# Kernel tuning notes

Hardware: AMD Instinct MI355X
Metric: run time of the kernel (lower is better)

## Reference

```python
import jax, jax.numpy as jnp
import numpy as np

B, S, D, K = 8, 2048, 1024, 204  # K = int(0.1 * seq_len)
LN_EPS = 1e-12


def setup_inputs() -> dict:
    key = jax.random.key(0)
    ks = jax.random.split(key, 8)
    scale = 0.02
    return {
        "input_tensor": jax.random.normal(ks[0], (B, S, D), jnp.float32),
        "attention_mask": jnp.zeros((B, 1, 1, S), jnp.float32),  # unused by module
        "Wq": jax.random.normal(ks[1], (D, K), jnp.float32) * scale,
        "bq": jnp.zeros((K,), jnp.float32),
        "Wk": jax.random.normal(ks[2], (D, K), jnp.float32) * scale,
        "bk": jnp.zeros((K,), jnp.float32),
        "Wv": jax.random.normal(ks[3], (D, D), jnp.float32) * scale,
        "bv": jnp.zeros((D,), jnp.float32),
        "Wd": jax.random.normal(ks[4], (D, D), jnp.float32) * scale,
        "bd": jnp.zeros((D,), jnp.float32),
        "gamma": jnp.ones((D,), jnp.float32),
        "beta": jnp.zeros((D,), jnp.float32),
    }


def reference(input_tensor, attention_mask, Wq, bq, Wk, bk, Wv, bv, Wd, bd, gamma, beta):
    # factorized synthesizer: low-rank (k=204) Q/K projections
    q = input_tensor @ Wq + bq          # [B,S,K]
    k = input_tensor @ Wk + bk          # [B,S,K]
    v = input_tensor @ Wv + bv          # [B,S,D]
    scores = jnp.einsum('bsk,btk->bst', q, k)          # [B,S,S]
    probs = jax.nn.softmax(scores, axis=-1)
    # per-head matmul with broadcast probs == direct matmul on merged heads
    ctx = jnp.einsum('bst,btd->bsd', probs, v)          # [B,S,D]
    h = ctx @ Wd + bd
    y = h + input_tensor                                 # residual
    mean = jnp.mean(y, axis=-1, keepdims=True)
    var = jnp.mean(jnp.square(y - mean), axis=-1, keepdims=True)
    return gamma * (y - mean) / jnp.sqrt(var + LN_EPS) + beta
```

## Files before the change

kernel.cpp:

```cpp
#include <hip/hip_runtime.h>
#include <stdint.h>

#define BB 8
#define SS 2048
#define DD 1024
#define KREAL 204

typedef __attribute__((ext_vector_type(8))) short short8;
typedef __attribute__((ext_vector_type(4))) float floatx4;
typedef uint16_t u16;
typedef uint32_t u32;

__device__ __forceinline__ float bf2f(u16 u) {
    union { float f; u32 i; } c; c.i = ((u32)u) << 16; return c.f;
}
__device__ __forceinline__ u16 f2bf(float f) {
    union { float f; u32 i; } c; c.f = f;
    u32 i = c.i;
    u32 r = (i + 0x7FFFu + ((i >> 16) & 1u)) >> 16;
    return (u16)r;
}

#if defined(__has_builtin)
#if __has_builtin(__builtin_amdgcn_global_load_lds)
#define HAVE_GLL 1
#endif
#endif

__device__ __forceinline__ void gload16(const u16* g, u16* l) {
#ifdef HAVE_GLL
    __builtin_amdgcn_global_load_lds(
        (const __attribute__((address_space(1))) void*)(uintptr_t)g,
        (__attribute__((address_space(3))) void*)(u32)(uintptr_t)(void*)l,
        16, 0, 0);
#else
    *(uint4*)l = *(const uint4*)g;
#endif
}

#define VM_WAIT(N) asm volatile("s_waitcnt vmcnt(" #N ")" ::: "memory")
#define S_BAR()    asm volatile("s_barrier" ::: "memory")

__device__ __forceinline__ void stage64(const u16* __restrict__ src, size_t ld,
                                        u16* lds, int tid) {
#pragma unroll
    for (int j = 0; j < 2; j++) {
        int flat = j * 256 + tid;
        int row = flat >> 3, slot = flat & 7;
        int kg = slot ^ (row & 7);
        gload16(src + (size_t)row * ld + kg * 8, lds + flat * 8);
    }
}
__device__ __forceinline__ short8 frag(const u16* lds, int row, int kslot) {
    return *(const short8*)&lds[(row << 6) + (((kslot ^ (row & 7)) & 7) << 3)];
}

__device__ __forceinline__ short8 frag32(const u16* plane, int row, int ks) {
    return *(const short8*)&plane[(row << 5) + (((ks ^ ((row >> 1) & 3)) & 3) << 3)];
}

__device__ __forceinline__ void stage_half(const u16* s0, const u16* s1,
                                           u16* dp, int tid) {
    gload16(s0, dp + tid * 8);
    gload16(s1, dp + 4096 + tid * 8);
}

template <int MT, bool LOADB>
__device__ __forceinline__ void phase16(const u16* Apl, const u16* Bpl,
                                        int arow, int brow, int ln, int quad,
                                        short8 (&bv)[4], floatx4 (&acc)[8][4]) {
    short8 af[4];
#pragma unroll
    for (int i = 0; i < 4; i++) af[i] = frag32(Apl, arow + (MT + i) * 16 + ln, quad);
    if (LOADB) {
#pragma unroll
        for (int nt = 0; nt < 4; nt++) bv[nt] = frag32(Bpl, brow + nt * 16 + ln, quad);
    }
    __builtin_amdgcn_s_setprio(1);
#pragma unroll
    for (int i = 0; i < 4; i++)
#pragma unroll
        for (int nt = 0; nt < 4; nt++)
            acc[MT + i][nt] = __builtin_amdgcn_mfma_f32_16x16x32_bf16(
                af[i], bv[nt], acc[MT + i][nt], 0, 0, 0);
    __builtin_amdgcn_s_setprio(0);
}

template <int NT>
__device__ __forceinline__ void gemm_core256(
    const u16* __restrict__ Ag, size_t lda,
    const u16* __restrict__ Bg, size_t ldb,
    u16* lds, int tid, floatx4 (&acc)[8][4]) {
    const int lane = tid & 63, w = tid >> 6;
    const int arow = (w >> 2) * 128, brow = (w & 3) * 64;
    const int ln = lane & 15, quad = lane >> 4;
    const int srow = tid >> 2;
    const int kgp = (tid & 3) ^ ((srow >> 1) & 3);
    const u16* A0 = Ag + (size_t)srow * lda + kgp * 8;
    const u16* A1 = Ag + (size_t)(srow + 128) * lda + kgp * 8;
    const u16* B0 = Bg + (size_t)srow * ldb + kgp * 8;
    const u16* B1 = Bg + (size_t)(srow + 128) * ldb + kgp * 8;
    u16* Al = lds;
    u16* Bl = lds + 32768;

    stage_half(A0,      A1,      Al,         tid);
    stage_half(B0,      B1,      Bl,         tid);
    stage_half(A0 + 32, A1 + 32, Al + 8192,  tid);
    stage_half(B0 + 32, B1 + 32, Bl + 8192,  tid);
    stage_half(A0 + 64, A1 + 64, Al + 16384, tid);
    stage_half(B0 + 64, B1 + 64, Bl + 16384, tid);

    short8 bv[4];
#pragma unroll 2
    for (int t = 0; t < NT - 1; ++t) {
        const int p  = (t & 1) * 2;
        const int pn = 2 - p;
        const u16* Ap0 = Al + p * 8192;
        const u16* Ap1 = Al + p * 8192 + 8192;
        const u16* Bp0 = Bl + p * 8192;
        const u16* Bp1 = Bl + p * 8192 + 8192;
        const size_t o1 = (size_t)(t + 1) * 64;
        const size_t o2 = (size_t)(t + 2) * 64;
        VM_WAIT(8); S_BAR();
        stage_half(A0 + o1 + 32, A1 + o1 + 32, Al + (pn + 1) * 8192, tid);
        phase16<0, true >(Ap0, Bp0, arow, brow, ln, quad, bv, acc);
        stage_half(B0 + o1 + 32, B1 + o1 + 32, Bl + (pn + 1) * 8192, tid);
        phase16<4, false>(Ap0, Bp0, arow, brow, ln, quad, bv, acc);
        VM_WAIT(8); S_BAR();
        if (t + 2 < NT) stage_half(A0 + o2, A1 + o2, Al + p * 8192, tid);
        phase16<0, true >(Ap1, Bp1, arow, brow, ln, quad, bv, acc);
        if (t + 2 < NT) stage_half(B0 + o2, B1 + o2, Bl + p * 8192, tid);
        phase16<4, false>(Ap1, Bp1, arow, brow, ln, quad, bv, acc);
    }
    {
        const int p = ((NT - 1) & 1) * 2;
        const u16* Ap0 = Al + p * 8192;
        const u16* Ap1 = Al + p * 8192 + 8192;
        const u16* Bp0 = Bl + p * 8192;
        const u16* Bp1 = Bl + p * 8192 + 8192;
        VM_WAIT(4); S_BAR();
        phase16<0, true >(Ap0, Bp0, arow, brow, ln, quad, bv, acc);
        phase16<4, false>(Ap0, Bp0, arow, brow, ln, quad, bv, acc);
        VM_WAIT(0); S_BAR();
        phase16<0, true >(Ap1, Bp1, arow, brow, ln, quad, bv, acc);
        phase16<4, false>(Ap1, Bp1, arow, brow, ln, quad, bv, acc);
    }
}

template <typename F>
__device__ __forceinline__ void store_rm256(u16* smem, u16* gbase, size_t ldc,
                                            int wm, int wn, int ln, int quad,
                                            int tid, F val) {
    for (int half = 0; half < 2; half++) {
        __syncthreads();
        if (wm == half) {
#pragma unroll
            for (int mt = 0; mt < 8; mt++)
#pragma unroll
                for (int nt = 0; nt < 4; nt++)
#pragma unroll
                    for (int r = 0; r < 4; r++)
                        smem[(mt * 16 + quad * 4 + r) * 264 + wn * 64 + nt * 16 + ln] =
                            val(mt, nt, r);
        }
        __syncthreads();
#pragma unroll
        for (int j = 0; j < 8; j++) {
            int flat = j * 512 + tid;
            int row = flat >> 5, c = flat & 31;
            *(uint4*)&gbase[(size_t)(half * 128 + row) * ldc + c * 8] =
                *(const uint4*)&smem[row * 264 + c * 8];
        }
    }
}

template <typename F4>
__device__ __forceinline__ void store_tr256(u16* smem, u16* gbase, size_t ldg,
                                            int wm, int wn, int ln, int quad,
                                            int tid, F4 val4) {
    for (int qr = 0; qr < 4; qr++) {
        __syncthreads();
        if (wn == qr) {
#pragma unroll
            for (int mt = 0; mt < 8; mt++)
#pragma unroll
                for (int nt = 0; nt < 4; nt++) {
                    ushort4 v = val4(mt, nt);
                    *(ushort4*)&smem[(nt * 16 + ln) * 264 + wm * 128 + mt * 16 + quad * 4] = v;
                }
        }
        __syncthreads();
#pragma unroll
        for (int j = 0; j < 4; j++) {
            int flat = j * 512 + tid;
            int c = flat >> 5, r8 = flat & 31;
            *(uint4*)&gbase[(size_t)(qr * 64 + c) * ldg + r8 * 8] =
                *(const uint4*)&smem[c * 264 + r8 * 8];
        }
    }
}

__global__ __launch_bounds__(256) void k_cast_bf16(
    const float* __restrict__ x, u16* __restrict__ o) {
    size_t i = ((size_t)blockIdx.x * 256 + threadIdx.x) * 4;
    float4 v = *(const float4*)&x[i];
    ushort4 p;
    p.x = f2bf(v.x); p.y = f2bf(v.y); p.z = f2bf(v.z); p.w = f2bf(v.w);
    *(ushort4*)&o[i] = p;
}

__global__ __launch_bounds__(256) void k_prep(
    const float* __restrict__ Wq, const float* __restrict__ Wk,
    const float* __restrict__ Wv, const float* __restrict__ Wd,
    const float* __restrict__ bv, const float* __restrict__ bd,
    const float* __restrict__ bq, const float* __restrict__ bk,
    u16* __restrict__ Wqkt, u16* __restrict__ Wv16, u16* __restrict__ Wdt,
    float* __restrict__ bc, float* __restrict__ bqk) {
    const int z = blockIdx.z;
    const int t = threadIdx.x;
    if (z == 4) {
        int id = blockIdx.y * 32 + blockIdx.x;
        if (id < 16) {
            __shared__ float red[4][64];
            int n = id * 64 + (t & 63);
            int dc = t >> 6;
            float s = 0.f;
            for (int d = dc * 256; d < dc * 256 + 256; d++)
                s += bv[d] * Wd[(size_t)d * 1024 + n];
            red[dc][t & 63] = s;
            __syncthreads();
            if (dc == 0) bc[n] = bd[n] + red[0][t & 63] + red[1][t & 63] + red[2][t & 63] + red[3][t & 63];
        } else if (id == 16) {
            for (int i = t; i < 512; i += 256) {
                float v = 0.f;
                if (i < KREAL) v = bq[i];
                else if (i >= 256 && i < 256 + KREAL) v = bk[i - 256];
                bqk[i] = v;
            }
        }
        return;
    }
    __shared__ u16 tile[32][33];
    int k0 = blockIdx.x * 32, n0 = blockIdx.y * 32;
    int tx = t & 31, ty = t >> 5;
    if (z == 2) {
        for (int i = ty; i < 32; i += 8) {
            size_t idx = (size_t)(k0 + i) * 1024 + n0 + tx;
            Wv16[idx] = f2bf(Wv[idx]);
        }
        return;
    }
    const float* W; u16* out; int N, Npad, rowoff;
    if (z == 0)      { W = Wq; out = Wqkt; N = KREAL; Npad = 256;  rowoff = 0;   }
    else if (z == 1) { W = Wk; out = Wqkt; N = KREAL; Npad = 256;  rowoff = 256; }
    else             { W = Wd; out = Wdt;  N = 1024;  Npad = 1024; rowoff = 0;   }
    if (n0 >= Npad) return;
    for (int i = ty; i < 32; i += 8) {
        int n = n0 + tx;
        tile[i][tx] = (n < N) ? f2bf(W[(size_t)(k0 + i) * N + n]) : (u16)0;
    }
    __syncthreads();
    for (int i = ty; i < 32; i += 8) {
        int n = n0 + i;
        if (n < Npad) out[(size_t)(rowoff + n) * 1024 + k0 + tx] = tile[tx][i];
    }
}

__global__ __launch_bounds__(256) void k_gemm64(
    const u16* __restrict__ A, const u16* __restrict__ Bt,
    u16* __restrict__ C, int ldc) {
    __shared__ u16 As[64 * 64];
    __shared__ u16 Bs[64 * 64];
    const int tid = threadIdx.x;
    const int m0 = blockIdx.x * 64, n0 = blockIdx.y * 64;
    const int lane = tid & 63, w = tid >> 6;
    const int ln = lane & 15, quad = lane >> 4;

    floatx4 acc[4];
    floatx4 zero = {0.f, 0.f, 0.f, 0.f};
#pragma unroll
    for (int nt = 0; nt < 4; nt++) acc[nt] = zero;

    for (int kt = 0; kt < 16; kt++) {
        __syncthreads();
        stage64(A + (size_t)m0 * 1024 + kt * 64, 1024, As, tid);
        stage64(Bt + (size_t)n0 * 1024 + kt * 64, 1024, Bs, tid);
        __syncthreads();
#pragma unroll
        for (int kk = 0; kk < 2; kk++) {
            short8 av = frag(As, w * 16 + ln, kk * 4 + quad);
#pragma unroll
            for (int nt = 0; nt < 4; nt++) {
                short8 bvf = frag(Bs, nt * 16 + ln, kk * 4 + quad);
                acc[nt] = __builtin_amdgcn_mfma_f32_16x16x32_bf16(av, bvf, acc[nt], 0, 0, 0);
            }
        }
    }
    const int row0 = m0 + w * 16 + quad * 4;
#pragma unroll
    for (int nt = 0; nt < 4; nt++) {
        const int col = n0 + nt * 16 + ln;
        ushort4 pk;
        pk.x = f2bf(acc[nt][0]); pk.y = f2bf(acc[nt][1]);
        pk.z = f2bf(acc[nt][2]); pk.w = f2bf(acc[nt][3]);
        *reinterpret_cast<ushort4*>(&C[(size_t)col * ldc + row0]) = pk;
    }
}

__global__ __launch_bounds__(512, 2) void k_proj2(
    const u16* __restrict__ A, const u16* __restrict__ Wqkt,
    const u16* __restrict__ Wvdt, const float* __restrict__ bqk,
    u16* __restrict__ qkp, u16* __restrict__ ut) {
    __shared__ __align__(16) u16 lds[65536];
    const int tid = threadIdx.x;
    int lin = blockIdx.x + (blockIdx.y << 6);
    int l = (lin & 7) * 48 + (lin >> 3);
    const int by = l % 6;
    const int m0 = (l / 6) * 256;
    const int lane = tid & 63, w = tid >> 6;
    const int wm = w >> 2, wn = w & 3;
    const int ln = lane & 15, quad = lane >> 4;

    floatx4 acc[8][4];
    floatx4 zero = {0.f, 0.f, 0.f, 0.f};
#pragma unroll
    for (int mt = 0; mt < 8; mt++)
#pragma unroll
        for (int nt = 0; nt < 4; nt++) acc[mt][nt] = zero;

    const u16* Ag = A + (size_t)m0 * 1024;
    const int n0 = (by < 2) ? by * 256 : (by - 2) * 256;
    const u16* Bg = (by < 2) ? (Wqkt + (size_t)n0 * 1024) : (Wvdt + (size_t)n0 * 1024);
    gemm_core256<16>(Ag, 1024, Bg, 1024, lds, tid, acc);

    if (by < 2) {
        float b4[4];
#pragma unroll
        for (int nt = 0; nt < 4; nt++) b4[nt] = bqk[n0 + wn * 64 + nt * 16 + ln];
        store_rm256(lds, qkp + (size_t)m0 * 512 + n0, 512, wm, wn, ln, quad, tid,
            [&](int mt, int nt, int r) -> u16 {
                return f2bf(acc[mt][nt][r] + b4[nt]);
            });
    } else {
        int b = m0 >> 11, s0loc = m0 & 2047;
        store_tr256(lds, ut + ((size_t)b * DD + n0) * SS + s0loc, SS, wm, wn, ln, quad, tid,
            [&](int mt, int nt) -> ushort4 {
                ushort4 pk;
                pk.x = f2bf(acc[mt][nt][0]); pk.y = f2bf(acc[mt][nt][1]);
                pk.z = f2bf(acc[mt][nt][2]); pk.w = f2bf(acc[mt][nt][3]);
                return pk;
            });
    }
}

__global__ __launch_bounds__(512, 2) void k_qk2(
    const u16* __restrict__ qkp, u16* __restrict__ P, float* __restrict__ lg) {
    __shared__ __align__(16) u16 lds[65536];
    const int tid = threadIdx.x;
    int lin = blockIdx.x + (blockIdx.y << 3) + (blockIdx.z << 6);
    int l = ((lin & 7) << 6) + (lin >> 3);
    const int bb = l >> 6, rem = l & 63;
    const int s0 = (rem & 7) * 256, t0 = (rem >> 3) * 256;
    const int lane = tid & 63, w = tid >> 6;
    const int wm = w >> 2, wn = w & 3;
    const int ln = lane & 15, quad = lane >> 4;

    floatx4 acc[8][4];
    floatx4 zero = {0.f, 0.f, 0.f, 0.f};
#pragma unroll
    for (int mt = 0; mt < 8; mt++)
#pragma unroll
        for (int nt = 0; nt < 4; nt++) acc[mt][nt] = zero;

    gemm_core256<4>(qkp + ((size_t)bb * SS + s0) * 512, 512,
                    qkp + ((size_t)bb * SS + t0) * 512 + 256, 512, lds, tid, acc);

#pragma unroll
    for (int mt = 0; mt < 8; mt++)
#pragma unroll
        for (int nt = 0; nt < 4; nt++)
#pragma unroll
            for (int r = 0; r < 4; r++)
                acc[mt][nt][r] = __expf(acc[mt][nt][r] - 30.f);

#pragma unroll
    for (int mt = 0; mt < 8; mt++) {
#pragma unroll
        for (int r = 0; r < 4; r++) {
            float rs = acc[mt][0][r] + acc[mt][1][r] + acc[mt][2][r] + acc[mt][3][r];
            rs += __shfl_xor(rs, 1);
            rs += __shfl_xor(rs, 2);
            rs += __shfl_xor(rs, 4);
            rs += __shfl_xor(rs, 8);
            if (ln == 0)
                atomicAdd(&lg[(size_t)bb * SS + s0 + wm * 128 + mt * 16 + quad * 4 + r], rs);
        }
    }

    store_rm256(lds, P + (size_t)bb * SS * SS + (size_t)s0 * SS + t0, SS,
                wm, wn, ln, quad, tid,
        [&](int mt, int nt, int r) -> u16 { return f2bf(acc[mt][nt][r]); });
}

__global__ __launch_bounds__(512, 2) void k_h2(
    const u16* __restrict__ P, const u16* __restrict__ ut,
    const float* __restrict__ lg, const float* __restrict__ bc,
    const float* __restrict__ xres, float* __restrict__ out) {
    __shared__ __align__(16) u16 lds[65536];
    const int tid = threadIdx.x;
    int lin = blockIdx.x + (blockIdx.y << 3) + (blockIdx.z << 5);
    int l = ((lin & 7) << 5) + (lin >> 3);
    const int bb = l >> 5, rem = l & 31;
    const int s0 = (rem & 7) * 256, d0 = (rem >> 3) * 256;
    const int lane = tid & 63, w = tid >> 6;
    const int wm = w >> 2, wn = w & 3;
    const int ln = lane & 15, quad = lane >> 4;

    floatx4 acc[8][4];
    floatx4 zero = {0.f, 0.f, 0.f, 0.f};
#pragma unroll
    for (int mt = 0; mt < 8; mt++)
#pragma unroll
        for (int nt = 0; nt < 4; nt++) acc[mt][nt] = zero;

    gemm_core256<32>(P + ((size_t)bb * SS + s0) * SS, SS,
                     ut + ((size_t)bb * DD + d0) * SS, SS, lds, tid, acc);

    float* smem = (float*)lds;
    float* outb = out + ((size_t)bb * SS + s0) * DD + d0;
    const float* xb = xres + ((size_t)bb * SS + s0) * DD + d0;
    for (int c4 = 0; c4 < 4; c4++) {
        __syncthreads();
        if (wm == (c4 >> 1)) {
#pragma unroll
            for (int i = 0; i < 4; i++)
#pragma unroll
                for (int nt = 0; nt < 4; nt++)
#pragma unroll
                    for (int r = 0; r < 4; r++)
                        smem[(i * 16 + quad * 4 + r) * 260 + wn * 64 + nt * 16 + ln] =
                            acc[(c4 & 1) * 4 + i][nt][r];
        }
        __syncthreads();
#pragma unroll
        for (int j = 0; j < 8; j++) {
            int flat = j * 512 + tid;
            int row = flat >> 6, q = flat & 63;
            size_t grow = (size_t)bb * SS + s0 + c4 * 64 + row;
            float iv = 1.f / lg[grow];
            float4 a  = *(const float4*)&smem[row * 260 + q * 4];
            float4 b4 = *(const float4*)&bc[d0 + q * 4];
            float4 xr = *(const float4*)&xb[(size_t)(c4 * 64 + row) * DD + q * 4];
            float4 o;
            o.x = a.x * iv + b4.x + xr.x;
            o.y = a.y * iv + b4.y + xr.y;
            o.z = a.z * iv + b4.z + xr.z;
            o.w = a.w * iv + b4.w + xr.w;
            *(float4*)&outb[(size_t)(c4 * 64 + row) * DD + q * 4] = o;
        }
    }
}

__global__ __launch_bounds__(256) void k_ln_f32(
    float* __restrict__ io, const float* __restrict__ gamma,
    const float* __restrict__ beta) {
    const int tid = threadIdx.x;
    const int lane = tid & 63, w = tid >> 6;
    const size_t row = (size_t)blockIdx.x * 4 + w;
    float* rp = io + row * DD;

    float v[16];
#pragma unroll
    for (int j = 0; j < 4; j++) {
        float4 t = *(const float4*)&rp[j * 256 + lane * 4];
        v[j * 4 + 0] = t.x; v[j * 4 + 1] = t.y; v[j * 4 + 2] = t.z; v[j * 4 + 3] = t.w;
    }
    float s = 0.f, sq = 0.f;
#pragma unroll
    for (int i = 0; i < 16; i++) { s += v[i]; sq += v[i] * v[i]; }
#pragma unroll
    for (int msk = 1; msk < 64; msk <<= 1) {
        s  += __shfl_xor(s,  msk, 64);
        sq += __shfl_xor(sq, msk, 64);
    }
    float mean = s * (1.f / 1024.f);
    float var  = sq * (1.f / 1024.f) - mean * mean;
    float rstd = rsqrtf(fmaxf(var, 0.f) + 1e-12f);
#pragma unroll
    for (int j = 0; j < 4; j++) {
        float4 g  = *(const float4*)&gamma[j * 256 + lane * 4];
        float4 bt = *(const float4*)&beta [j * 256 + lane * 4];
        float4 o;
        o.x = g.x * (v[j * 4 + 0] - mean) * rstd + bt.x;
        o.y = g.y * (v[j * 4 + 1] - mean) * rstd + bt.y;
        o.z = g.z * (v[j * 4 + 2] - mean) * rstd + bt.z;
        o.w = g.w * (v[j * 4 + 3] - mean) * rstd + bt.w;
        *(float4*)&rp[j * 256 + lane * 4] = o;
    }
}

extern "C" void kernel_launch(void* const* d_in, const int* in_sizes, int n_in,
                              void* d_out, int out_size, void* d_ws, size_t ws_size,
                              hipStream_t stream) {
    const float* x     = (const float*)d_in[0];
    const float* Wq    = (const float*)d_in[2];
    const float* bq    = (const float*)d_in[3];
    const float* Wk    = (const float*)d_in[4];
    const float* bk    = (const float*)d_in[5];
    const float* Wv    = (const float*)d_in[6];
    const float* bv    = (const float*)d_in[7];
    const float* Wd    = (const float*)d_in[8];
    const float* bd    = (const float*)d_in[9];
    const float* gamma = (const float*)d_in[10];
    const float* beta  = (const float*)d_in[11];
    float* out = (float*)d_out;

    char* ws = (char*)d_ws;
    u16*   qkp  = (u16*)(ws + 0);
    u16*   ut   = (u16*)(ws + 16777216);
    u16*   P    = (u16*)(ws + 50331648);
    u16*   x16  = (u16*)(ws + 50331648);
    u16*   Wv16 = (u16*)(ws + 83886080);
    u16*   Wvdt = (u16*)(ws + 85983232);
    u16*   Wdt  = (u16*)(ws + 88080384);
    u16*   Wqkt = (u16*)(ws + 90177536);
    float* lg   = (float*)(ws + 117440512);
    float* bc   = (float*)(ws + 117506048);
    float* bqk  = (float*)(ws + 117510144);

    k_cast_bf16<<<dim3(16384), dim3(256), 0, stream>>>(x, x16);
    k_prep<<<dim3(32, 32, 5), dim3(256), 0, stream>>>(Wq, Wk, Wv, Wd, bv, bd, bq, bk,
                                                      Wqkt, Wv16, Wdt, bc, bqk);
    k_gemm64<<<dim3(16, 16), dim3(256), 0, stream>>>(Wv16, Wdt, Wvdt, 1024);

    k_proj2<<<dim3(64, 6), dim3(512), 0, stream>>>(x16, Wqkt, Wvdt, bqk, qkp, ut);

    hipMemsetAsync(lg, 0, (size_t)BB * SS * sizeof(float), stream);

    k_qk2<<<dim3(8, 8, 8), dim3(512), 0, stream>>>(qkp, P, lg);
    k_h2 <<<dim3(8, 4, 8), dim3(512), 0, stream>>>(P, ut, lg, bc, x, out);

    k_ln_f32<<<dim3(4096), dim3(256), 0, stream>>>(out, gamma, beta);
}
```

Baseline: 428.5 us.

## Shrink P·V tile to 256x128, batch-split QK/PV launches, drop block swizzles

```diff
diff --git a/kernel.cpp b/kernel.cpp
--- a/kernel.cpp
+++ b/kernel.cpp
@@ -59,40 +59,37 @@
     return *(const short8*)&plane[(row << 5) + (((ks ^ ((row >> 1) & 3)) & 3) << 3)];
 }
 
-__device__ __forceinline__ void stage_half(const u16* s0, const u16* s1,
-                                           u16* dp, int tid) {
-    gload16(s0, dp + tid * 8);
-    gload16(s1, dp + 4096 + tid * 8);
-}
-
-template <int MT, bool LOADB>
-__device__ __forceinline__ void phase16(const u16* Apl, const u16* Bpl,
-                                        int arow, int brow, int ln, int quad,
-                                        short8 (&bv)[4], floatx4 (&acc)[8][4]) {
-    short8 af[4];
-#pragma unroll
-    for (int i = 0; i < 4; i++) af[i] = frag32(Apl, arow + (MT + i) * 16 + ln, quad);
+template <int MT0, int MTN, int MTOT, bool LOADB>
+__device__ __forceinline__ void phaseN(const u16* Apl, const u16* Bpl,
+                                       int arow, int brow, int ln, int quad,
+                                       short8 (&bv)[4], floatx4 (&acc)[MTOT][4]) {
+    short8 af[MTN];
+#pragma unroll
+    for (int i = 0; i < MTN; i++) af[i] = frag32(Apl, arow + (MT0 + i) * 16 + ln, quad);
     if (LOADB) {
 #pragma unroll
         for (int nt = 0; nt < 4; nt++) bv[nt] = frag32(Bpl, brow + nt * 16 + ln, quad);
     }
     __builtin_amdgcn_s_setprio(1);
 #pragma unroll
-    for (int i = 0; i < 4; i++)
+    for (int i = 0; i < MTN; i++)
 #pragma unroll
         for (int nt = 0; nt < 4; nt++)
-            acc[MT + i][nt] = __builtin_amdgcn_mfma_f32_16x16x32_bf16(
-                af[i], bv[nt], acc[MT + i][nt], 0, 0, 0);
+            acc[MT0 + i][nt] = __builtin_amdgcn_mfma_f32_16x16x32_bf16(
+                af[i], bv[nt], acc[MT0 + i][nt], 0, 0, 0);
     __builtin_amdgcn_s_setprio(0);
 }
 
-template <int NT>
-__device__ __forceinline__ void gemm_core256(
+template <int NT, int NB, int MTOT>
+__device__ __forceinline__ void gemm_core(
     const u16* __restrict__ Ag, size_t lda,
     const u16* __restrict__ Bg, size_t ldb,
-    u16* lds, int tid, floatx4 (&acc)[8][4]) {
+    u16* lds, int tid, floatx4 (&acc)[MTOT][4]) {
+    constexpr int BPL = NB * 32;
+    constexpr int MH = MTOT / 2;
     const int lane = tid & 63, w = tid >> 6;
-    const int arow = (w >> 2) * 128, brow = (w & 3) * 64;
+    const int arow = (NB == 256) ? (w >> 2) * 128 : (w >> 1) * 64;
+    const int brow = (NB == 256) ? (w & 3) * 64  : (w & 1) * 64;
     const int ln = lane & 15, quad = lane >> 4;
     const int srow = tid >> 2;
     const int kgp = (tid & 3) ^ ((srow >> 1) & 3);
@@ -101,49 +98,54 @@
     const u16* B0 = Bg + (size_t)srow * ldb + kgp * 8;
     const u16* B1 = Bg + (size_t)(srow + 128) * ldb + kgp * 8;
     u16* Al = lds;
-    u16* Bl = lds + 32768;
-
-    stage_half(A0,      A1,      Al,         tid);
-    stage_half(B0,      B1,      Bl,         tid);
-    stage_half(A0 + 32, A1 + 32, Al + 8192,  tid);
-    stage_half(B0 + 32, B1 + 32, Bl + 8192,  tid);
-    stage_half(A0 + 64, A1 + 64, Al + 16384, tid);
-    stage_half(B0 + 64, B1 + 64, Bl + 16384, tid);
+    u16* Bl = lds + 4 * 8192;
+
+    auto stageA = [&](size_t koff, int plane) {
+        gload16(A0 + koff, Al + plane * 8192 + tid * 8);
+        gload16(A1 + koff, Al + plane * 8192 + 4096 + tid * 8);
+    };
+    auto stageB = [&](size_t koff, int plane) {
+        gload16(B0 + koff, Bl + plane * BPL + tid * 8);
+        if constexpr (NB == 256)
+            gload16(B1 + koff, Bl + plane * BPL + 4096 + tid * 8);
+    };
+
+    stageA(0, 0);  stageB(0, 0);
+    stageA(32, 1); stageB(32, 1);
+    stageA(64, 2); stageB(64, 2);
 
     short8 bv[4];
 #pragma unroll 2
     for (int t = 0; t < NT - 1; ++t) {
-        const int p  = (t & 1) * 2;
-        const int pn = 2 - p;
-        const u16* Ap0 = Al + p * 8192;
-        const u16* Ap1 = Al + p * 8192 + 8192;
-        const u16* Bp0 = Bl + p * 8192;
-        const u16* Bp1 = Bl + p * 8192 + 8192;
+        const int p = (t & 1) * 2, pn = 2 - p;
+        const u16* Ap0 = Al + p * 8192;  const u16* Ap1 = Ap0 + 8192;
+        const u16* Bp0 = Bl + p * BPL;   const u16* Bp1 = Bp0 + BPL;
         const size_t o1 = (size_t)(t + 1) * 64;
         const size_t o2 = (size_t)(t + 2) * 64;
-        VM_WAIT(8); S_BAR();
-        stage_half(A0 + o1 + 32, A1 + o1 + 32, Al + (pn + 1) * 8192, tid);
-        phase16<0, true >(Ap0, Bp0, arow, brow, ln, quad, bv, acc);
-        stage_half(B0 + o1 + 32, B1 + o1 + 32, Bl + (pn + 1) * 8192, tid);
-        phase16<4, false>(Ap0, Bp0, arow, brow, ln, quad, bv, acc);
-        VM_WAIT(8); S_BAR();
-        if (t + 2 < NT) stage_half(A0 + o2, A1 + o2, Al + p * 8192, tid);
-        phase16<0, true >(Ap1, Bp1, arow, brow, ln, quad, bv, acc);
-        if (t + 2 < NT) stage_half(B0 + o2, B1 + o2, Bl + p * 8192, tid);
-        phase16<4, false>(Ap1, Bp1, arow, brow, ln, quad, bv, acc);
+        if constexpr (NB == 256) { VM_WAIT(8); } else { VM_WAIT(6); }
+        S_BAR();
+        stageA(o1 + 32, pn + 1);
+        phaseN<0, MH, MTOT, true >(Ap0, Bp0, arow, brow, ln, quad, bv, acc);
+        stageB(o1 + 32, pn + 1);
+        phaseN<MH, MH, MTOT, false>(Ap0, Bp0, arow, brow, ln, quad, bv, acc);
+        if constexpr (NB == 256) { VM_WAIT(8); } else { VM_WAIT(6); }
+        S_BAR();
+        if (t + 2 < NT) stageA(o2, p);
+        phaseN<0, MH, MTOT, true >(Ap1, Bp1, arow, brow, ln, quad, bv, acc);
+        if (t + 2 < NT) stageB(o2, p);
+        phaseN<MH, MH, MTOT, false>(Ap1, Bp1, arow, brow, ln, quad, bv, acc);
     }
     {
         const int p = ((NT - 1) & 1) * 2;
-        const u16* Ap0 = Al + p * 8192;
-        const u16* Ap1 = Al + p * 8192 + 8192;
-        const u16* Bp0 = Bl + p * 8192;
-        const u16* Bp1 = Bl + p * 8192 + 8192;
-        VM_WAIT(4); S_BAR();
-        phase16<0, true >(Ap0, Bp0, arow, brow, ln, quad, bv, acc);
-        phase16<4, false>(Ap0, Bp0, arow, brow, ln, quad, bv, acc);
+        const u16* Ap0 = Al + p * 8192;  const u16* Ap1 = Ap0 + 8192;
+        const u16* Bp0 = Bl + p * BPL;   const u16* Bp1 = Bp0 + BPL;
+        if constexpr (NB == 256) { VM_WAIT(4); } else { VM_WAIT(3); }
+        S_BAR();
+        phaseN<0, MH, MTOT, true >(Ap0, Bp0, arow, brow, ln, quad, bv, acc);
+        phaseN<MH, MH, MTOT, false>(Ap0, Bp0, arow, brow, ln, quad, bv, acc);
         VM_WAIT(0); S_BAR();
-        phase16<0, true >(Ap1, Bp1, arow, brow, ln, quad, bv, acc);
-        phase16<4, false>(Ap1, Bp1, arow, brow, ln, quad, bv, acc);
+        phaseN<0, MH, MTOT, true >(Ap1, Bp1, arow, brow, ln, quad, bv, acc);
+        phaseN<MH, MH, MTOT, false>(Ap1, Bp1, arow, brow, ln, quad, bv, acc);
     }
 }
 
@@ -313,10 +315,8 @@
     u16* __restrict__ qkp, u16* __restrict__ ut) {
     __shared__ __align__(16) u16 lds[65536];
     const int tid = threadIdx.x;
-    int lin = blockIdx.x + (blockIdx.y << 6);
-    int l = (lin & 7) * 48 + (lin >> 3);
-    const int by = l % 6;
-    const int m0 = (l / 6) * 256;
+    const int m0 = blockIdx.x * 256;
+    const int by = blockIdx.y;
     const int lane = tid & 63, w = tid >> 6;
     const int wm = w >> 2, wn = w & 3;
     const int ln = lane & 15, quad = lane >> 4;
@@ -331,7 +331,7 @@
     const u16* Ag = A + (size_t)m0 * 1024;
     const int n0 = (by < 2) ? by * 256 : (by - 2) * 256;
     const u16* Bg = (by < 2) ? (Wqkt + (size_t)n0 * 1024) : (Wvdt + (size_t)n0 * 1024);
-    gemm_core256<16>(Ag, 1024, Bg, 1024, lds, tid, acc);
+    gemm_core<16, 256, 8>(Ag, 1024, Bg, 1024, lds, tid, acc);
 
     if (by < 2) {
         float b4[4];
@@ -357,10 +357,7 @@
     const u16* __restrict__ qkp, u16* __restrict__ P, float* __restrict__ lg) {
     __shared__ __align__(16) u16 lds[65536];
     const int tid = threadIdx.x;
-    int lin = blockIdx.x + (blockIdx.y << 3) + (blockIdx.z << 6);
-    int l = ((lin & 7) << 6) + (lin >> 3);
-    const int bb = l >> 6, rem = l & 63;
-    const int s0 = (rem & 7) * 256, t0 = (rem >> 3) * 256;
+    const int s0 = blockIdx.x * 256, t0 = blockIdx.y * 256, bb = blockIdx.z;
     const int lane = tid & 63, w = tid >> 6;
     const int wm = w >> 2, wn = w & 3;
     const int ln = lane & 15, quad = lane >> 4;
@@ -372,8 +369,8 @@
 #pragma unroll
         for (int nt = 0; nt < 4; nt++) acc[mt][nt] = zero;
 
-    gemm_core256<4>(qkp + ((size_t)bb * SS + s0) * 512, 512,
-                    qkp + ((size_t)bb * SS + t0) * 512 + 256, 512, lds, tid, acc);
+    gemm_core<4, 256, 8>(qkp + ((size_t)bb * SS + s0) * 512, 512,
+                         qkp + ((size_t)bb * SS + t0) * 512 + 256, 512, lds, tid, acc);
 
 #pragma unroll
     for (int mt = 0; mt < 8; mt++)
@@ -402,53 +399,49 @@
         [&](int mt, int nt, int r) -> u16 { return f2bf(acc[mt][nt][r]); });
 }
 
-__global__ __launch_bounds__(512, 2) void k_h2(
+__global__ __launch_bounds__(512, 2) void k_h3(
     const u16* __restrict__ P, const u16* __restrict__ ut,
     const float* __restrict__ lg, const float* __restrict__ bc,
     const float* __restrict__ xres, float* __restrict__ out) {
-    __shared__ __align__(16) u16 lds[65536];
+    __shared__ __align__(16) u16 lds[49152];
     const int tid = threadIdx.x;
-    int lin = blockIdx.x + (blockIdx.y << 3) + (blockIdx.z << 5);
-    int l = ((lin & 7) << 5) + (lin >> 3);
-    const int bb = l >> 5, rem = l & 31;
-    const int s0 = (rem & 7) * 256, d0 = (rem >> 3) * 256;
+    const int s0 = blockIdx.x * 256, d0 = blockIdx.y * 128, bb = blockIdx.z;
     const int lane = tid & 63, w = tid >> 6;
-    const int wm = w >> 2, wn = w & 3;
     const int ln = lane & 15, quad = lane >> 4;
 
-    floatx4 acc[8][4];
+    floatx4 acc[4][4];
     floatx4 zero = {0.f, 0.f, 0.f, 0.f};
 #pragma unroll
-    for (int mt = 0; mt < 8; mt++)
+    for (int mt = 0; mt < 4; mt++)
 #pragma unroll
         for (int nt = 0; nt < 4; nt++) acc[mt][nt] = zero;
 
-    gemm_core256<32>(P + ((size_t)bb * SS + s0) * SS, SS,
-                     ut + ((size_t)bb * DD + d0) * SS, SS, lds, tid, acc);
+    gemm_core<32, 128, 4>(P + ((size_t)bb * SS + s0) * SS, SS,
+                          ut + ((size_t)bb * DD + d0) * SS, SS, lds, tid, acc);
 
     float* smem = (float*)lds;
     float* outb = out + ((size_t)bb * SS + s0) * DD + d0;
     const float* xb = xres + ((size_t)bb * SS + s0) * DD + d0;
+    const float* lgb = lg + (size_t)bb * SS + s0;
     for (int c4 = 0; c4 < 4; c4++) {
         __syncthreads();
-        if (wm == (c4 >> 1)) {
-#pragma unroll
-            for (int i = 0; i < 4; i++)
+        if ((w >> 1) == c4) {
+#pragma unroll
+            for (int mt = 0; mt < 4; mt++)
 #pragma unroll
                 for (int nt = 0; nt < 4; nt++)
 #pragma unroll
                     for (int r = 0; r < 4; r++)
-                        smem[(i * 16 + quad * 4 + r) * 260 + wn * 64 + nt * 16 + ln] =
-                            acc[(c4 & 1) * 4 + i][nt][r];
-        }
-        __syncthreads();
-#pragma unroll
-        for (int j = 0; j < 8; j++) {
+                        smem[(mt * 16 + quad * 4 + r) * 132 + (w & 1) * 64 + nt * 16 + ln] =
+                            acc[mt][nt][r];
+        }
+        __syncthreads();
+#pragma unroll
+        for (int j = 0; j < 4; j++) {
             int flat = j * 512 + tid;
-            int row = flat >> 6, q = flat & 63;
-            size_t grow = (size_t)bb * SS + s0 + c4 * 64 + row;
-            float iv = 1.f / lg[grow];
-            float4 a  = *(const float4*)&smem[row * 260 + q * 4];
+            int row = flat >> 5, q = flat & 31;
+            float iv = 1.f / lgb[c4 * 64 + row];
+            float4 a  = *(const float4*)&smem[row * 132 + q * 4];
             float4 b4 = *(const float4*)&bc[d0 + q * 4];
             float4 xr = *(const float4*)&xb[(size_t)(c4 * 64 + row) * DD + q * 4];
             float4 o;
@@ -537,8 +530,14 @@
 
     hipMemsetAsync(lg, 0, (size_t)BB * SS * sizeof(float), stream);
 
-    k_qk2<<<dim3(8, 8, 8), dim3(512), 0, stream>>>(qkp, P, lg);
-    k_h2 <<<dim3(8, 4, 8), dim3(512), 0, stream>>>(P, ut, lg, bc, x, out);
+    for (int g = 0; g < 2; g++) {
+        const size_t qo = (size_t)g * 4 * SS * 512;
+        const size_t uo = (size_t)g * 4 * (size_t)DD * SS;
+        const size_t xo = (size_t)g * 4 * (size_t)SS * DD;
+        const size_t lo = (size_t)g * 4 * SS;
+        k_qk2<<<dim3(8, 8, 4), dim3(512), 0, stream>>>(qkp + qo, P, lg + lo);
+        k_h3 <<<dim3(8, 8, 4), dim3(512), 0, stream>>>(P, ut + uo, lg + lo, bc, x + xo, out + xo);
+    }
 
     k_ln_f32<<<dim3(4096), dim3(256), 0, stream>>>(out, gamma, beta);
 }
```

Measured after the change: 372.5 us. 13.1% less time.

## Switch GEMM core to a five-slot LDS ring with deeper prefetch

Applied to the files above, without the earlier changes.

```diff
diff --git a/kernel.cpp b/kernel.cpp
--- a/kernel.cpp
+++ b/kernel.cpp
@@ -59,19 +59,13 @@
     return *(const short8*)&plane[(row << 5) + (((ks ^ ((row >> 1) & 3)) & 3) << 3)];
 }
 
-__device__ __forceinline__ void stage_half(const u16* s0, const u16* s1,
-                                           u16* dp, int tid) {
-    gload16(s0, dp + tid * 8);
-    gload16(s1, dp + 4096 + tid * 8);
-}
-
-template <int MT, bool LOADB>
+template <int MT0, bool LOADB>
 __device__ __forceinline__ void phase16(const u16* Apl, const u16* Bpl,
                                         int arow, int brow, int ln, int quad,
                                         short8 (&bv)[4], floatx4 (&acc)[8][4]) {
     short8 af[4];
 #pragma unroll
-    for (int i = 0; i < 4; i++) af[i] = frag32(Apl, arow + (MT + i) * 16 + ln, quad);
+    for (int i = 0; i < 4; i++) af[i] = frag32(Apl, arow + (MT0 + i) * 16 + ln, quad);
     if (LOADB) {
 #pragma unroll
         for (int nt = 0; nt < 4; nt++) bv[nt] = frag32(Bpl, brow + nt * 16 + ln, quad);
@@ -81,16 +75,17 @@
     for (int i = 0; i < 4; i++)
 #pragma unroll
         for (int nt = 0; nt < 4; nt++)
-            acc[MT + i][nt] = __builtin_amdgcn_mfma_f32_16x16x32_bf16(
-                af[i], bv[nt], acc[MT + i][nt], 0, 0, 0);
+            acc[MT0 + i][nt] = __builtin_amdgcn_mfma_f32_16x16x32_bf16(
+                af[i], bv[nt], acc[MT0 + i][nt], 0, 0, 0);
     __builtin_amdgcn_s_setprio(0);
 }
 
 template <int NT>
-__device__ __forceinline__ void gemm_core256(
+__device__ __forceinline__ void gemm_core5(
     const u16* __restrict__ Ag, size_t lda,
     const u16* __restrict__ Bg, size_t ldb,
     u16* lds, int tid, floatx4 (&acc)[8][4]) {
+    static_assert(NT >= 3, "ring-5 core needs NT >= 3");
     const int lane = tid & 63, w = tid >> 6;
     const int arow = (w >> 2) * 128, brow = (w & 3) * 64;
     const int ln = lane & 15, quad = lane >> 4;
@@ -101,43 +96,51 @@
     const u16* B0 = Bg + (size_t)srow * ldb + kgp * 8;
     const u16* B1 = Bg + (size_t)(srow + 128) * ldb + kgp * 8;
     u16* Al = lds;
-    u16* Bl = lds + 32768;
-
-    stage_half(A0,      A1,      Al,         tid);
-    stage_half(B0,      B1,      Bl,         tid);
-    stage_half(A0 + 32, A1 + 32, Al + 8192,  tid);
-    stage_half(B0 + 32, B1 + 32, Bl + 8192,  tid);
-    stage_half(A0 + 64, A1 + 64, Al + 16384, tid);
-    stage_half(B0 + 64, B1 + 64, Bl + 16384, tid);
+    u16* Bl = lds + 5 * 8192;
+
+    auto SH = [&](int sl, int h) {
+        size_t koff = (size_t)h * 32;
+        gload16(A0 + koff, Al + sl * 8192 + tid * 8);
+        gload16(A1 + koff, Al + sl * 8192 + 4096 + tid * 8);
+        gload16(B0 + koff, Bl + sl * 8192 + tid * 8);
+        gload16(B1 + koff, Bl + sl * 8192 + 4096 + tid * 8);
+    };
+
+    SH(0, 0); SH(1, 1); SH(2, 2); SH(3, 3);
 
     short8 bv[4];
+    int sl0 = 0, sl1 = 1;
 #pragma unroll 2
-    for (int t = 0; t < NT - 1; ++t) {
-        const int p  = (t & 1) * 2;
-        const int pn = 2 - p;
-        const u16* Ap0 = Al + p * 8192;
-        const u16* Ap1 = Al + p * 8192 + 8192;
-        const u16* Bp0 = Bl + p * 8192;
-        const u16* Bp1 = Bl + p * 8192 + 8192;
-        const size_t o1 = (size_t)(t + 1) * 64;
-        const size_t o2 = (size_t)(t + 2) * 64;
-        VM_WAIT(8); S_BAR();
-        stage_half(A0 + o1 + 32, A1 + o1 + 32, Al + (pn + 1) * 8192, tid);
+    for (int t = 0; t < NT - 2; ++t) {
+        const u16* Ap0 = Al + sl0 * 8192;  const u16* Bp0 = Bl + sl0 * 8192;
+        const u16* Ap1 = Al + sl1 * 8192;  const u16* Bp1 = Bl + sl1 * 8192;
+        const int st = sl0 ? sl0 - 1 : 4;
+        VM_WAIT(12); S_BAR();
+        SH(st, 2 * t + 4);
         phase16<0, true >(Ap0, Bp0, arow, brow, ln, quad, bv, acc);
-        stage_half(B0 + o1 + 32, B1 + o1 + 32, Bl + (pn + 1) * 8192, tid);
+        phase16<4, false>(Ap0, Bp0, arow, brow, ln, quad, bv, acc);
+        VM_WAIT(12); S_BAR();
+        SH(sl0, 2 * t + 5);
+        phase16<0, true >(Ap1, Bp1, arow, brow, ln, quad, bv, acc);
+        phase16<4, false>(Ap1, Bp1, arow, brow, ln, quad, bv, acc);
+        sl0 += 2; if (sl0 >= 5) sl0 -= 5;
+        sl1 += 2; if (sl1 >= 5) sl1 -= 5;
+    }
+    {
+        const u16* Ap0 = Al + sl0 * 8192;  const u16* Bp0 = Bl + sl0 * 8192;
+        const u16* Ap1 = Al + sl1 * 8192;  const u16* Bp1 = Bl + sl1 * 8192;
+        VM_WAIT(12); S_BAR();
+        phase16<0, true >(Ap0, Bp0, arow, brow, ln, quad, bv, acc);
         phase16<4, false>(Ap0, Bp0, arow, brow, ln, quad, bv, acc);
         VM_WAIT(8); S_BAR();
-        if (t + 2 < NT) stage_half(A0 + o2, A1 + o2, Al + p * 8192, tid);
         phase16<0, true >(Ap1, Bp1, arow, brow, ln, quad, bv, acc);
-        if (t + 2 < NT) stage_half(B0 + o2, B1 + o2, Bl + p * 8192, tid);
         phase16<4, false>(Ap1, Bp1, arow, brow, ln, quad, bv, acc);
+        sl0 += 2; if (sl0 >= 5) sl0 -= 5;
+        sl1 += 2; if (sl1 >= 5) sl1 -= 5;
     }
     {
-        const int p = ((NT - 1) & 1) * 2;
-        const u16* Ap0 = Al + p * 8192;
-        const u16* Ap1 = Al + p * 8192 + 8192;
-        const u16* Bp0 = Bl + p * 8192;
-        const u16* Bp1 = Bl + p * 8192 + 8192;
+        const u16* Ap0 = Al + sl0 * 8192;  const u16* Bp0 = Bl + sl0 * 8192;
+        const u16* Ap1 = Al + sl1 * 8192;  const u16* Bp1 = Bl + sl1 * 8192;
         VM_WAIT(4); S_BAR();
         phase16<0, true >(Ap0, Bp0, arow, brow, ln, quad, bv, acc);
         phase16<4, false>(Ap0, Bp0, arow, brow, ln, quad, bv, acc);
@@ -311,12 +314,10 @@
     const u16* __restrict__ A, const u16* __restrict__ Wqkt,
     const u16* __restrict__ Wvdt, const float* __restrict__ bqk,
     u16* __restrict__ qkp, u16* __restrict__ ut) {
-    __shared__ __align__(16) u16 lds[65536];
+    __shared__ __align__(16) u16 lds[81920];
     const int tid = threadIdx.x;
-    int lin = blockIdx.x + (blockIdx.y << 6);
-    int l = (lin & 7) * 48 + (lin >> 3);
-    const int by = l % 6;
-    const int m0 = (l / 6) * 256;
+    const int m0 = blockIdx.x * 256;
+    const int by = blockIdx.y;
     const int lane = tid & 63, w = tid >> 6;
     const int wm = w >> 2, wn = w & 3;
     const int ln = lane & 15, quad = lane >> 4;
@@ -331,7 +332,7 @@
     const u16* Ag = A + (size_t)m0 * 1024;
     const int n0 = (by < 2) ? by * 256 : (by - 2) * 256;
     const u16* Bg = (by < 2) ? (Wqkt + (size_t)n0 * 1024) : (Wvdt + (size_t)n0 * 1024);
-    gemm_core256<16>(Ag, 1024, Bg, 1024, lds, tid, acc);
+    gemm_core5<16>(Ag, 1024, Bg, 1024, lds, tid, acc);
 
     if (by < 2) {
         float b4[4];
@@ -355,12 +356,9 @@
 
 __global__ __launch_bounds__(512, 2) void k_qk2(
     const u16* __restrict__ qkp, u16* __restrict__ P, float* __restrict__ lg) {
-    __shared__ __align__(16) u16 lds[65536];
+    __shared__ __align__(16) u16 lds[81920];
     const int tid = threadIdx.x;
-    int lin = blockIdx.x + (blockIdx.y << 3) + (blockIdx.z << 6);
-    int l = ((lin & 7) << 6) + (lin >> 3);
-    const int bb = l >> 6, rem = l & 63;
-    const int s0 = (rem & 7) * 256, t0 = (rem >> 3) * 256;
+    const int s0 = blockIdx.x * 256, t0 = blockIdx.y * 256, bb = blockIdx.z;
     const int lane = tid & 63, w = tid >> 6;
     const int wm = w >> 2, wn = w & 3;
     const int ln = lane & 15, quad = lane >> 4;
@@ -372,8 +370,8 @@
 #pragma unroll
         for (int nt = 0; nt < 4; nt++) acc[mt][nt] = zero;
 
-    gemm_core256<4>(qkp + ((size_t)bb * SS + s0) * 512, 512,
-                    qkp + ((size_t)bb * SS + t0) * 512 + 256, 512, lds, tid, acc);
+    gemm_core5<4>(qkp + ((size_t)bb * SS + s0) * 512, 512,
+                  qkp + ((size_t)bb * SS + t0) * 512 + 256, 512, lds, tid, acc);
 
 #pragma unroll
     for (int mt = 0; mt < 8; mt++)
@@ -406,14 +404,11 @@
     const u16* __restrict__ P, const u16* __restrict__ ut,
     const float* __restrict__ lg, const float* __restrict__ bc,
     const float* __restrict__ xres, float* __restrict__ out) {
-    __shared__ __align__(16) u16 lds[65536];
+    __shared__ __align__(16) u16 lds[81920];
     const int tid = threadIdx.x;
-    int lin = blockIdx.x + (blockIdx.y << 3) + (blockIdx.z << 5);
-    int l = ((lin & 7) << 5) + (lin >> 3);
-    const int bb = l >> 5, rem = l & 31;
-    const int s0 = (rem & 7) * 256, d0 = (rem >> 3) * 256;
+    const int s0 = blockIdx.x * 256, d0 = blockIdx.y * 256, bb = blockIdx.z;
     const int lane = tid & 63, w = tid >> 6;
-    const int wm = w >> 2, wn = w & 3;
+    const int wm = w >> 2;
     const int ln = lane & 15, quad = lane >> 4;
 
     floatx4 acc[8][4];
@@ -423,12 +418,14 @@
 #pragma unroll
         for (int nt = 0; nt < 4; nt++) acc[mt][nt] = zero;
 
-    gemm_core256<32>(P + ((size_t)bb * SS + s0) * SS, SS,
-                     ut + ((size_t)bb * DD + d0) * SS, SS, lds, tid, acc);
+    gemm_core5<32>(P + ((size_t)bb * SS + s0) * SS, SS,
+                   ut + ((size_t)bb * DD + d0) * SS, SS, lds, tid, acc);
 
     float* smem = (float*)lds;
     float* outb = out + ((size_t)bb * SS + s0) * DD + d0;
     const float* xb = xres + ((size_t)bb * SS + s0) * DD + d0;
+    const float* lgb = lg + (size_t)bb * SS + s0;
+    const int wn = w & 3;
     for (int c4 = 0; c4 < 4; c4++) {
         __syncthreads();
         if (wm == (c4 >> 1)) {
@@ -446,8 +443,7 @@
         for (int j = 0; j < 8; j++) {
             int flat = j * 512 + tid;
             int row = flat >> 6, q = flat & 63;
-            size_t grow = (size_t)bb * SS + s0 + c4 * 64 + row;
-            float iv = 1.f / lg[grow];
+            float iv = 1.f / lgb[c4 * 64 + row];
             float4 a  = *(const float4*)&smem[row * 260 + q * 4];
             float4 b4 = *(const float4*)&bc[d0 + q * 4];
             float4 xr = *(const float4*)&xb[(size_t)(c4 * 64 + row) * DD + q * 4];
```

Result: faster. 358.4 us (-16.4%).
